# Performance work log

Hardware: AMD Instinct MI355X
Metric: run time of the kernel (lower is better)

Reference implementation:

```python
import jax, jax.numpy as jnp
import numpy as np

N_NODES = 100000
N_EDGES = 1600000
IN_C, HID_C, OUT_C = 128, 128, 64


def gcn_conv(x, W, b, src, dst, n_nodes):
    """PyG-style GCNConv: h = x @ W; add self-loops; symmetric deg^-1/2 norm;
    scatter-add aggregation; + bias. Self-loop contribution added analytically
    (norm for self-loop edge i->i is deg_i^-1) instead of materializing edges."""
    h = x @ W  # [N, C_out]
    # degree over dst including self-loops (edge weights are all ones)
    deg = jax.ops.segment_sum(jnp.ones((src.shape[0],), h.dtype), dst,
                              num_segments=n_nodes) + 1.0
    dinv = jax.lax.rsqrt(deg)  # deg >= 1 always
    norm = dinv[src] * dinv[dst]  # [E]
    agg = jax.ops.segment_sum(h[src] * norm[:, None], dst, num_segments=n_nodes)
    agg = agg + h * (dinv * dinv)[:, None]  # self-loop term
    return agg + b


def setup_inputs() -> dict:
    key = jax.random.key(0)
    k0, k1, k2, k3, k4, k5 = jax.random.split(key, 6)
    x = jax.random.normal(k0, (N_NODES, IN_C), dtype=jnp.float32)
    edge_index = jax.random.randint(k1, (2, N_EDGES), 0, N_NODES, dtype=jnp.int64)
    s1 = 1.0 / np.sqrt(IN_C)
    s2 = 1.0 / np.sqrt(HID_C)
    W1 = jax.random.uniform(k2, (IN_C, HID_C), jnp.float32, -s1, s1)
    b1 = jax.random.uniform(k3, (HID_C,), jnp.float32, -s1, s1)
    W2 = jax.random.uniform(k4, (HID_C, OUT_C), jnp.float32, -s2, s2)
    b2 = jax.random.uniform(k5, (OUT_C,), jnp.float32, -s2, s2)
    return {"x": x, "W1": W1, "b1": b1, "W2": W2, "b2": b2,
            "edge_index": edge_index}


def reference(x, W1, b1, W2, b2, edge_index):
    src, dst = edge_index[0], edge_index[1]
    h = gcn_conv(x, W1, b1, src, dst, N_NODES)
    h = jax.nn.relu(h)
    out = gcn_conv(h, W2, b2, src, dst, N_NODES)
    return out
```

## Files before the change

kernel.cpp:

```cpp
#include <hip/hip_runtime.h>


static constexpr int BSHIFT = 7;
static constexpr int BWIDTH = 1 << BSHIFT;
static constexpr int MAXBUCK = 2048;
static constexpr int NPART = 256;

static constexpr size_t OFF_FLAG = 0;
static constexpr size_t OFF_DEG  = 256;
static constexpr size_t OFF_ROW  = 458752;
static constexpr size_t OFF_BSUM = 917504;
static constexpr size_t OFF_CCNT = 925696;
static constexpr size_t OFF_COFF = 937984;
static constexpr size_t OFF_DINV = 962560;
static constexpr size_t OFF_CSR  = 1376256;
static constexpr size_t OFF_HS1  = 8388608;
static constexpr size_t OFF_OUT1 = 35651584;
static constexpr size_t OFF_HS2  = 62914560;
static constexpr size_t OFF_H2   = 75714560;

__device__ __forceinline__ unsigned short f2bf(float f) {
    unsigned u = __float_as_uint(f);
    u += 0x7fffu + ((u >> 16) & 1u);
    return (unsigned short)(u >> 16);
}

typedef __attribute__((ext_vector_type(8))) short bf16x8;
typedef __attribute__((ext_vector_type(4))) float f32x4;

__global__ void detect_kernel(const unsigned* __restrict__ w,
                              unsigned* __restrict__ flag) {
    int i = blockIdx.x * blockDim.x + threadIdx.x;
    if (w[2 * i + 1] != 0u) atomicOr(flag, 1u);
}

__device__ __forceinline__ int edge_dst(const unsigned* w, unsigned flag,
                                        int e, int E) {
    return flag ? (int)w[E + e] : (int)w[2 * E + 2 * e];
}
__device__ __forceinline__ int edge_src(const unsigned* w, unsigned flag,
                                        int e, int E) {
    return flag ? (int)w[e] : (int)w[2 * e];
}

__global__ __launch_bounds__(1024) void coarse_hist_kernel(
    const unsigned* __restrict__ w, const unsigned* __restrict__ flag,
    unsigned* __restrict__ ccnt, unsigned* __restrict__ h2, int E, int nbuck) {
    __shared__ unsigned hist[MAXBUCK];
    for (int i = threadIdx.x; i < nbuck; i += 1024) hist[i] = 0;
    __syncthreads();
    const unsigned f = *flag;
    const int per = (E + gridDim.x - 1) / gridDim.x;
    const int e0 = blockIdx.x * per, e1 = min(E, e0 + per);
    for (int e = e0 + (int)threadIdx.x; e < e1; e += 1024)
        atomicAdd(&hist[edge_dst(w, f, e, E) >> BSHIFT], 1u);
    __syncthreads();
    for (int i = threadIdx.x; i < nbuck; i += 1024) {
        unsigned h = hist[i];
        h2[(size_t)i * NPART + blockIdx.x] = h;
        if (h) atomicAdd(&ccnt[i], h);
    }
}

__global__ __launch_bounds__(1024) void coarse_scan_kernel(
    const unsigned* __restrict__ ccnt, unsigned* __restrict__ coff, int nbuck) {
    __shared__ unsigned sh[1024];
    const int t = threadIdx.x;
    unsigned run = 0;
    for (int b0 = 0; b0 < nbuck; b0 += 1024) {
        unsigned v = (b0 + t < nbuck) ? ccnt[b0 + t] : 0u;
        sh[t] = v;
        __syncthreads();
        for (int off = 1; off < 1024; off <<= 1) {
            unsigned a = (t >= off) ? sh[t - off] : 0u;
            __syncthreads();
            sh[t] += a;
            __syncthreads();
        }
        if (b0 + t < nbuck) coff[b0 + t] = run + sh[t] - v;
        run += sh[1023];
        __syncthreads();
    }
    if (t == 0) coff[nbuck] = run;
}

__global__ __launch_bounds__(NPART) void off2d_kernel(
    unsigned* __restrict__ h2, const unsigned* __restrict__ coff) {
    __shared__ unsigned sh[NPART];
    const int b = blockIdx.x, t = threadIdx.x;
    unsigned v = h2[(size_t)b * NPART + t];
    sh[t] = v;
    __syncthreads();
#pragma unroll
    for (int off = 1; off < NPART; off <<= 1) {
        unsigned a = (t >= off) ? sh[t - off] : 0u;
        __syncthreads();
        sh[t] += a;
        __syncthreads();
    }
    h2[(size_t)b * NPART + t] = coff[b] + sh[t] - v;
}

__global__ __launch_bounds__(1024) void partition_kernel(
    const unsigned* __restrict__ w, const unsigned* __restrict__ flag,
    const unsigned* __restrict__ h2, unsigned* __restrict__ part, int E,
    int nbuck) {
    __shared__ unsigned lcur[MAXBUCK];
    for (int i = threadIdx.x; i < nbuck; i += 1024)
        lcur[i] = h2[(size_t)i * NPART + blockIdx.x];
    __syncthreads();
    const unsigned f = *flag;
    const int per = (E + gridDim.x - 1) / gridDim.x;
    const int e0 = blockIdx.x * per, e1 = min(E, e0 + per);
    for (int e = e0 + (int)threadIdx.x; e < e1; e += 1024) {
        int d = edge_dst(w, f, e, E);
        int s = edge_src(w, f, e, E);
        unsigned pos = atomicAdd(&lcur[d >> BSHIFT], 1u);
        part[pos] = (unsigned)s | ((unsigned)(d & (BWIDTH - 1)) << 20);
    }
}

__global__ __launch_bounds__(256) void bucket_csr_kernel(
    const unsigned* __restrict__ part, const unsigned* __restrict__ coff,
    unsigned* __restrict__ deg, int* __restrict__ csr, int N) {
    __shared__ unsigned cnt[BWIDTH];
    __shared__ unsigned sc[BWIDTH];
    __shared__ unsigned cur[BWIDTH];
    const int b = blockIdx.x, base = b << BSHIFT, t = threadIdx.x;
    if (t < BWIDTH) cnt[t] = 0;
    __syncthreads();
    const int e0 = (int)coff[b], e1 = (int)coff[b + 1];
    for (int e = e0 + t; e < e1; e += 256)
        atomicAdd(&cnt[part[e] >> 20], 1u);
    __syncthreads();
    if (t < BWIDTH && base + t < N) deg[base + t] = cnt[t];
    if (t < BWIDTH) sc[t] = cnt[t];
    __syncthreads();
#pragma unroll
    for (int off = 1; off < BWIDTH; off <<= 1) {
        unsigned a = (t < BWIDTH && t >= off) ? sc[t - off] : 0u;
        __syncthreads();
        if (t < BWIDTH) sc[t] += a;
        __syncthreads();
    }
    if (t < BWIDTH) cur[t] = (unsigned)e0 + sc[t] - cnt[t];
    __syncthreads();
    for (int e = e0 + t; e < e1; e += 256) {
        unsigned pk = part[e];
        unsigned p = atomicAdd(&cur[pk >> 20], 1u);
        csr[p] = (int)(pk & 0xFFFFFu);
    }
}

__global__ __launch_bounds__(1024) void scan1_kernel(
    const unsigned* __restrict__ deg, unsigned* __restrict__ row,
    unsigned* __restrict__ bsum, int N) {
    __shared__ unsigned sh[1024];
    int gid = blockIdx.x * 1024 + threadIdx.x;
    int t = threadIdx.x;
    unsigned v = (gid < N) ? deg[gid] : 0u;
    sh[t] = v;
    __syncthreads();
#pragma unroll
    for (int off = 1; off < 1024; off <<= 1) {
        unsigned add = (t >= off) ? sh[t - off] : 0u;
        __syncthreads();
        sh[t] += add;
        __syncthreads();
    }
    if (gid < N) row[gid + 1] = sh[t];
    if (t == 1023) bsum[blockIdx.x] = sh[1023];
}

__global__ __launch_bounds__(1024) void scan2_kernel(unsigned* __restrict__ bsum,
                                                     int NB) {
    __shared__ unsigned sh[1024];
    const int t = threadIdx.x;
    unsigned v = (t < NB) ? bsum[t] : 0u;
    sh[t] = v;
    __syncthreads();
#pragma unroll
    for (int off = 1; off < 1024; off <<= 1) {
        unsigned a = (t >= off) ? sh[t - off] : 0u;
        __syncthreads();
        sh[t] += a;
        __syncthreads();
    }
    if (t < NB) bsum[t] = sh[t] - v;
}

__global__ void scan3_kernel(unsigned* __restrict__ row,
                             const unsigned* __restrict__ bsum,
                             const unsigned* __restrict__ deg,
                             float* __restrict__ dinv, int N) {
    int gid = blockIdx.x * blockDim.x + threadIdx.x;
    if (gid >= N) return;
    row[gid + 1] += bsum[gid >> 10];
    if (gid == 0) row[0] = 0u;
    dinv[gid] = rsqrtf((float)deg[gid] + 1.0f);
}

template <int BN, bool ABF16>
__global__ __launch_bounds__(256) void gemm_mfma(
    const void* __restrict__ Av, const float* __restrict__ B,
    const float* __restrict__ dinv, unsigned short* __restrict__ out, int M) {
    constexpr int NT = BN / 16;
    __shared__ short sA[16384];
    __shared__ short sB[NT * 2048];

    const int t = threadIdx.x;
    const int row0 = blockIdx.x * 128;
    const int w = t >> 6, lane = t & 63;
    const int m = lane & 15, q = lane >> 4;

    if (ABF16) {
        const unsigned short* A = (const unsigned short*)Av;
        for (int g = t; g < 2048; g += 256) {
            int r = g >> 4, k0 = (g & 15) << 3;
            uint4 v = make_uint4(0u, 0u, 0u, 0u);
            if (row0 + r < M) v = *(const uint4*)(A + (size_t)(row0 + r) * 128 + k0);
            int off = ((((r >> 4) * 4 + (k0 >> 5)) * 16 + (r & 15)) * 4 +
                       ((k0 >> 3) & 3)) * 8;
            *(uint4*)(sA + off) = v;
        }
    } else {
        const float* A = (const float*)Av;
        for (int g = t; g < 4096; g += 256) {
            int r = g >> 5, k0 = (g & 31) << 2;
            float4 v = make_float4(0.f, 0.f, 0.f, 0.f);
            if (row0 + r < M) v = *(const float4*)(A + (size_t)(row0 + r) * 128 + k0);
            ushort4 u;
            u.x = f2bf(v.x); u.y = f2bf(v.y); u.z = f2bf(v.z); u.w = f2bf(v.w);
            int off = ((((r >> 4) * 4 + (k0 >> 5)) * 16 + (r & 15)) * 4 +
                       ((k0 >> 3) & 3)) * 8 + (k0 & 4);
            *(ushort4*)(sA + off) = u;
        }
    }
    for (int g = t; g < BN * 32; g += 256) {
        int n = g % BN, k0 = (g / BN) * 4;
        float f0 = B[(size_t)(k0 + 0) * BN + n];
        float f1 = B[(size_t)(k0 + 1) * BN + n];
        float f2 = B[(size_t)(k0 + 2) * BN + n];
        float f3 = B[(size_t)(k0 + 3) * BN + n];
        ushort4 u;
        u.x = f2bf(f0); u.y = f2bf(f1); u.z = f2bf(f2); u.w = f2bf(f3);
        int off = ((((n >> 4) * 4 + (k0 >> 5)) * 16 + (n & 15)) * 4 +
                   ((k0 >> 3) & 3)) * 8 + (k0 & 4);
        *(ushort4*)(sB + off) = u;
    }
    __syncthreads();

    f32x4 acc[2][NT];
#pragma unroll
    for (int lt = 0; lt < 2; lt++)
#pragma unroll
        for (int nt = 0; nt < NT; nt++) acc[lt][nt] = (f32x4){0.f, 0.f, 0.f, 0.f};

    const int fb = (m * 4 + q) * 8;
#pragma unroll
    for (int ks = 0; ks < 4; ks++) {
        bf16x8 a0 = *(const bf16x8*)(sA + ((w * 2 + 0) * 4 + ks) * 512 + fb);
        bf16x8 a1 = *(const bf16x8*)(sA + ((w * 2 + 1) * 4 + ks) * 512 + fb);
#pragma unroll
        for (int nt = 0; nt < NT; nt++) {
            bf16x8 b = *(const bf16x8*)(sB + (nt * 4 + ks) * 512 + fb);
            acc[0][nt] = __builtin_amdgcn_mfma_f32_16x16x32_bf16(a0, b, acc[0][nt], 0, 0, 0);
            acc[1][nt] = __builtin_amdgcn_mfma_f32_16x16x32_bf16(a1, b, acc[1][nt], 0, 0, 0);
        }
    }

#pragma unroll
    for (int lt = 0; lt < 2; lt++) {
#pragma unroll
        for (int r = 0; r < 4; r++) {
            int row = row0 + w * 32 + lt * 16 + q * 4 + r;
            if (row < M) {
                float s = dinv[row];
#pragma unroll
                for (int nt = 0; nt < NT; nt++)
                    out[(size_t)row * BN + nt * 16 + m] = f2bf(acc[lt][nt][r] * s);
            }
        }
    }
}

template <int C, bool RELU, bool OUTBF>
__global__ __launch_bounds__(256) void agg_kernel(
    const int* __restrict__ csr, const unsigned* __restrict__ row,
    const unsigned short* __restrict__ hsb, const float* __restrict__ dinv,
    const float* __restrict__ bias, void* __restrict__ outv, int N) {
    constexpr int LPN = C / 8;
    const int tid = blockIdx.x * 256 + threadIdx.x;
    const int i = tid / LPN;
    const int l = tid % LPN;
    if (i >= N) return;

    const int co = 8 * l;
    float s0 = 0.f, s1 = 0.f, s2 = 0.f, s3 = 0.f,
          s4 = 0.f, s5 = 0.f, s6 = 0.f, s7 = 0.f;
    {
        uint4 u = *(const uint4*)(hsb + (size_t)i * C + co);
        s0 += __uint_as_float(u.x << 16); s1 += __uint_as_float(u.x & 0xffff0000u);
        s2 += __uint_as_float(u.y << 16); s3 += __uint_as_float(u.y & 0xffff0000u);
        s4 += __uint_as_float(u.z << 16); s5 += __uint_as_float(u.z & 0xffff0000u);
        s6 += __uint_as_float(u.w << 16); s7 += __uint_as_float(u.w & 0xffff0000u);
    }

    const int rs = (int)row[i], re = (int)row[i + 1];
    for (int e0 = rs; e0 < re; e0 += LPN) {
        int idx = (e0 + l < re) ? csr[e0 + l] : 0;
        const int cnt = min(LPN, re - e0);
#pragma unroll 4
        for (int j = 0; j < cnt; j++) {
            int s = __shfl(idx, j, LPN);
            uint4 u = *(const uint4*)(hsb + (size_t)s * C + co);
            s0 += __uint_as_float(u.x << 16); s1 += __uint_as_float(u.x & 0xffff0000u);
            s2 += __uint_as_float(u.y << 16); s3 += __uint_as_float(u.y & 0xffff0000u);
            s4 += __uint_as_float(u.z << 16); s5 += __uint_as_float(u.z & 0xffff0000u);
            s6 += __uint_as_float(u.w << 16); s7 += __uint_as_float(u.w & 0xffff0000u);
        }
    }

    const float sc = dinv[i];
    const float4 ba = *(const float4*)(bias + co);
    const float4 bb = *(const float4*)(bias + co + 4);
    float o0 = s0 * sc + ba.x, o1 = s1 * sc + ba.y;
    float o2 = s2 * sc + ba.z, o3 = s3 * sc + ba.w;
    float o4 = s4 * sc + bb.x, o5 = s5 * sc + bb.y;
    float o6 = s6 * sc + bb.z, o7 = s7 * sc + bb.w;
    if (RELU) {
        o0 = fmaxf(o0, 0.f); o1 = fmaxf(o1, 0.f); o2 = fmaxf(o2, 0.f);
        o3 = fmaxf(o3, 0.f); o4 = fmaxf(o4, 0.f); o5 = fmaxf(o5, 0.f);
        o6 = fmaxf(o6, 0.f); o7 = fmaxf(o7, 0.f);
    }
    if (OUTBF) {
        uint4 u;
        u.x = (unsigned)f2bf(o0) | ((unsigned)f2bf(o1) << 16);
        u.y = (unsigned)f2bf(o2) | ((unsigned)f2bf(o3) << 16);
        u.z = (unsigned)f2bf(o4) | ((unsigned)f2bf(o5) << 16);
        u.w = (unsigned)f2bf(o6) | ((unsigned)f2bf(o7) << 16);
        *(uint4*)((unsigned short*)outv + (size_t)i * C + co) = u;
    } else {
        float4 a = make_float4(o0, o1, o2, o3);
        float4 b = make_float4(o4, o5, o6, o7);
        *(float4*)((float*)outv + (size_t)i * C + co) = a;
        *(float4*)((float*)outv + (size_t)i * C + co + 4) = b;
    }
}

extern "C" void kernel_launch(void* const* d_in, const int* in_sizes, int n_in,
                              void* d_out, int out_size, void* d_ws,
                              size_t ws_size, hipStream_t stream) {
    const float* x  = (const float*)d_in[0];
    const float* W1 = (const float*)d_in[1];
    const float* b1 = (const float*)d_in[2];
    const float* W2 = (const float*)d_in[3];
    const float* b2 = (const float*)d_in[4];
    const unsigned* ew = (const unsigned*)d_in[5];
    const int E = in_sizes[5] / 2;
    const int N = in_sizes[0] / 128;
    const int NB = (N + 1023) >> 10;
    const int nbuck = (N + BWIDTH - 1) >> BSHIFT;

    char* ws = (char*)d_ws;
    unsigned* flag = (unsigned*)(ws + OFF_FLAG);
    unsigned* deg  = (unsigned*)(ws + OFF_DEG);
    unsigned* row  = (unsigned*)(ws + OFF_ROW);
    unsigned* bsum = (unsigned*)(ws + OFF_BSUM);
    unsigned* ccnt = (unsigned*)(ws + OFF_CCNT);
    unsigned* coff = (unsigned*)(ws + OFF_COFF);
    float* dinv    = (float*)(ws + OFF_DINV);
    int* csr       = (int*)(ws + OFF_CSR);
    unsigned short* hs1  = (unsigned short*)(ws + OFF_HS1);
    unsigned short* out1 = (unsigned short*)(ws + OFF_OUT1);
    unsigned short* hs2  = (unsigned short*)(ws + OFF_HS2);
    unsigned* h2   = (unsigned*)(ws + OFF_H2);
    unsigned* part = (unsigned*)(ws + OFF_HS1);

    hipMemsetAsync(flag, 0, 4, stream);
    hipMemsetAsync(ccnt, 0, (size_t)(nbuck + 1) * 4, stream);

    detect_kernel<<<16, 256, 0, stream>>>(ew, flag);
    coarse_hist_kernel<<<NPART, 1024, 0, stream>>>(ew, flag, ccnt, h2, E, nbuck);
    coarse_scan_kernel<<<1, 1024, 0, stream>>>(ccnt, coff, nbuck);
    off2d_kernel<<<nbuck, NPART, 0, stream>>>(h2, coff);
    partition_kernel<<<NPART, 1024, 0, stream>>>(ew, flag, h2, part, E, nbuck);
    bucket_csr_kernel<<<nbuck, 256, 0, stream>>>(part, coff, deg, csr, N);
    scan1_kernel<<<NB, 1024, 0, stream>>>(deg, row, bsum, N);
    scan2_kernel<<<1, 1024, 0, stream>>>(bsum, NB);
    scan3_kernel<<<(N + 255) / 256, 256, 0, stream>>>(row, bsum, deg, dinv, N);

    gemm_mfma<128, false><<<(N + 127) / 128, 256, 0, stream>>>(x, W1, dinv, hs1, N);
    agg_kernel<128, true, true><<<(N * 16 + 255) / 256, 256, 0, stream>>>(
        csr, row, hs1, dinv, b1, out1, N);

    gemm_mfma<64, true><<<(N + 127) / 128, 256, 0, stream>>>(out1, W2, dinv, hs2, N);
    agg_kernel<64, false, false><<<(N * 8 + 255) / 256, 256, 0, stream>>>(
        csr, row, hs2, dinv, b2, d_out, N);
}
```

Before: 317.6 us.

## Slice feature tables into 16-column groups and fold scans into bucket CSR

Intermediate feature tables are stored channel-sliced (16 columns per slice), and aggregation blocks each gather one slice for 128 nodes, so each pass over the neighbour rows touches a smaller working set that fits in cache better. The GEMM loads its A fragments directly into registers instead of staging them in shared memory. The separate detect kernel and the three scan kernels are removed: the edge-index format is detected per block with __syncthreads_or, and row offsets and dinv are written inside bucket_csr_kernel. This saves several launches, but CSR row reads are repeated once per slice and the gather now moves 32-byte pieces instead of full rows.

```diff
diff --git a/kernel.cpp b/kernel.cpp
--- a/kernel.cpp
+++ b/kernel.cpp
@@ -6,14 +6,11 @@
 static constexpr int MAXBUCK = 2048;
 static constexpr int NPART = 256;
 
-static constexpr size_t OFF_FLAG = 0;
-static constexpr size_t OFF_DEG  = 256;
-static constexpr size_t OFF_ROW  = 458752;
-static constexpr size_t OFF_BSUM = 917504;
-static constexpr size_t OFF_CCNT = 925696;
-static constexpr size_t OFF_COFF = 937984;
-static constexpr size_t OFF_DINV = 962560;
-static constexpr size_t OFF_CSR  = 1376256;
+static constexpr size_t OFF_ROW  = 0;
+static constexpr size_t OFF_CCNT = 524288;
+static constexpr size_t OFF_COFF = 540672;
+static constexpr size_t OFF_DINV = 557056;
+static constexpr size_t OFF_CSR  = 1048576;
 static constexpr size_t OFF_HS1  = 8388608;
 static constexpr size_t OFF_OUT1 = 35651584;
 static constexpr size_t OFF_HS2  = 62914560;
@@ -28,10 +25,11 @@
 typedef __attribute__((ext_vector_type(8))) short bf16x8;
 typedef __attribute__((ext_vector_type(4))) float f32x4;
 
-__global__ void detect_kernel(const unsigned* __restrict__ w,
-                              unsigned* __restrict__ flag) {
-    int i = blockIdx.x * blockDim.x + threadIdx.x;
-    if (w[2 * i + 1] != 0u) atomicOr(flag, 1u);
+__device__ __forceinline__ void acc8(const uint4 u, float* s) {
+    s[0] += __uint_as_float(u.x << 16); s[1] += __uint_as_float(u.x & 0xffff0000u);
+    s[2] += __uint_as_float(u.y << 16); s[3] += __uint_as_float(u.y & 0xffff0000u);
+    s[4] += __uint_as_float(u.z << 16); s[5] += __uint_as_float(u.z & 0xffff0000u);
+    s[6] += __uint_as_float(u.w << 16); s[7] += __uint_as_float(u.w & 0xffff0000u);
 }
 
 __device__ __forceinline__ int edge_dst(const unsigned* w, unsigned flag,
@@ -42,16 +40,21 @@
                                         int e, int E) {
     return flag ? (int)w[e] : (int)w[2 * e];
 }
+__device__ __forceinline__ unsigned detect_local(const unsigned* w, int e0,
+                                                 int e1) {
+    int si = e0 + (int)threadIdx.x;
+    int pred = (si < e1) ? (w[2 * si + 1] != 0u) : 0;
+    return (unsigned)(__syncthreads_or(pred) != 0);
+}
 
 __global__ __launch_bounds__(1024) void coarse_hist_kernel(
-    const unsigned* __restrict__ w, const unsigned* __restrict__ flag,
-    unsigned* __restrict__ ccnt, unsigned* __restrict__ h2, int E, int nbuck) {
+    const unsigned* __restrict__ w, unsigned* __restrict__ ccnt,
+    unsigned* __restrict__ h2, int E, int nbuck) {
     __shared__ unsigned hist[MAXBUCK];
     for (int i = threadIdx.x; i < nbuck; i += 1024) hist[i] = 0;
-    __syncthreads();
-    const unsigned f = *flag;
     const int per = (E + gridDim.x - 1) / gridDim.x;
     const int e0 = blockIdx.x * per, e1 = min(E, e0 + per);
+    const unsigned f = detect_local(w, e0, e1);
     for (int e = e0 + (int)threadIdx.x; e < e1; e += 1024)
         atomicAdd(&hist[edge_dst(w, f, e, E) >> BSHIFT], 1u);
     __syncthreads();
@@ -102,16 +105,14 @@
 }
 
 __global__ __launch_bounds__(1024) void partition_kernel(
-    const unsigned* __restrict__ w, const unsigned* __restrict__ flag,
-    const unsigned* __restrict__ h2, unsigned* __restrict__ part, int E,
-    int nbuck) {
+    const unsigned* __restrict__ w, const unsigned* __restrict__ h2,
+    unsigned* __restrict__ part, int E, int nbuck) {
     __shared__ unsigned lcur[MAXBUCK];
     for (int i = threadIdx.x; i < nbuck; i += 1024)
         lcur[i] = h2[(size_t)i * NPART + blockIdx.x];
-    __syncthreads();
-    const unsigned f = *flag;
     const int per = (E + gridDim.x - 1) / gridDim.x;
     const int e0 = blockIdx.x * per, e1 = min(E, e0 + per);
+    const unsigned f = detect_local(w, e0, e1);
     for (int e = e0 + (int)threadIdx.x; e < e1; e += 1024) {
         int d = edge_dst(w, f, e, E);
         int s = edge_src(w, f, e, E);
@@ -122,7 +123,8 @@
 
 __global__ __launch_bounds__(256) void bucket_csr_kernel(
     const unsigned* __restrict__ part, const unsigned* __restrict__ coff,
-    unsigned* __restrict__ deg, int* __restrict__ csr, int N) {
+    unsigned* __restrict__ row, float* __restrict__ dinv,
+    int* __restrict__ csr, int N, int nbuck) {
     __shared__ unsigned cnt[BWIDTH];
     __shared__ unsigned sc[BWIDTH];
     __shared__ unsigned cur[BWIDTH];
@@ -133,7 +135,6 @@
     for (int e = e0 + t; e < e1; e += 256)
         atomicAdd(&cnt[part[e] >> 20], 1u);
     __syncthreads();
-    if (t < BWIDTH && base + t < N) deg[base + t] = cnt[t];
     if (t < BWIDTH) sc[t] = cnt[t];
     __syncthreads();
 #pragma unroll
@@ -143,7 +144,15 @@
         if (t < BWIDTH) sc[t] += a;
         __syncthreads();
     }
-    if (t < BWIDTH) cur[t] = (unsigned)e0 + sc[t] - cnt[t];
+    if (t < BWIDTH) {
+        unsigned ex = (unsigned)e0 + sc[t] - cnt[t];
+        cur[t] = ex;
+        if (base + t < N) {
+            row[base + t] = ex;
+            dinv[base + t] = rsqrtf((float)cnt[t] + 1.0f);
+        }
+    }
+    if (b == 0 && t == 0) row[N] = coff[nbuck];
     __syncthreads();
     for (int e = e0 + t; e < e1; e += 256) {
         unsigned pk = part[e];
@@ -152,60 +161,11 @@
     }
 }
 
-__global__ __launch_bounds__(1024) void scan1_kernel(
-    const unsigned* __restrict__ deg, unsigned* __restrict__ row,
-    unsigned* __restrict__ bsum, int N) {
-    __shared__ unsigned sh[1024];
-    int gid = blockIdx.x * 1024 + threadIdx.x;
-    int t = threadIdx.x;
-    unsigned v = (gid < N) ? deg[gid] : 0u;
-    sh[t] = v;
-    __syncthreads();
-#pragma unroll
-    for (int off = 1; off < 1024; off <<= 1) {
-        unsigned add = (t >= off) ? sh[t - off] : 0u;
-        __syncthreads();
-        sh[t] += add;
-        __syncthreads();
-    }
-    if (gid < N) row[gid + 1] = sh[t];
-    if (t == 1023) bsum[blockIdx.x] = sh[1023];
-}
-
-__global__ __launch_bounds__(1024) void scan2_kernel(unsigned* __restrict__ bsum,
-                                                     int NB) {
-    __shared__ unsigned sh[1024];
-    const int t = threadIdx.x;
-    unsigned v = (t < NB) ? bsum[t] : 0u;
-    sh[t] = v;
-    __syncthreads();
-#pragma unroll
-    for (int off = 1; off < 1024; off <<= 1) {
-        unsigned a = (t >= off) ? sh[t - off] : 0u;
-        __syncthreads();
-        sh[t] += a;
-        __syncthreads();
-    }
-    if (t < NB) bsum[t] = sh[t] - v;
-}
-
-__global__ void scan3_kernel(unsigned* __restrict__ row,
-                             const unsigned* __restrict__ bsum,
-                             const unsigned* __restrict__ deg,
-                             float* __restrict__ dinv, int N) {
-    int gid = blockIdx.x * blockDim.x + threadIdx.x;
-    if (gid >= N) return;
-    row[gid + 1] += bsum[gid >> 10];
-    if (gid == 0) row[0] = 0u;
-    dinv[gid] = rsqrtf((float)deg[gid] + 1.0f);
-}
-
 template <int BN, bool ABF16>
 __global__ __launch_bounds__(256) void gemm_mfma(
     const void* __restrict__ Av, const float* __restrict__ B,
-    const float* __restrict__ dinv, unsigned short* __restrict__ out, int M) {
+    const float* __restrict__ dinv, unsigned short* __restrict__ outg, int M) {
     constexpr int NT = BN / 16;
-    __shared__ short sA[16384];
     __shared__ short sB[NT * 2048];
 
     const int t = threadIdx.x;
@@ -213,29 +173,6 @@
     const int w = t >> 6, lane = t & 63;
     const int m = lane & 15, q = lane >> 4;
 
-    if (ABF16) {
-        const unsigned short* A = (const unsigned short*)Av;
-        for (int g = t; g < 2048; g += 256) {
-            int r = g >> 4, k0 = (g & 15) << 3;
-            uint4 v = make_uint4(0u, 0u, 0u, 0u);
-            if (row0 + r < M) v = *(const uint4*)(A + (size_t)(row0 + r) * 128 + k0);
-            int off = ((((r >> 4) * 4 + (k0 >> 5)) * 16 + (r & 15)) * 4 +
-                       ((k0 >> 3) & 3)) * 8;
-            *(uint4*)(sA + off) = v;
-        }
-    } else {
-        const float* A = (const float*)Av;
-        for (int g = t; g < 4096; g += 256) {
-            int r = g >> 5, k0 = (g & 31) << 2;
-            float4 v = make_float4(0.f, 0.f, 0.f, 0.f);
-            if (row0 + r < M) v = *(const float4*)(A + (size_t)(row0 + r) * 128 + k0);
-            ushort4 u;
-            u.x = f2bf(v.x); u.y = f2bf(v.y); u.z = f2bf(v.z); u.w = f2bf(v.w);
-            int off = ((((r >> 4) * 4 + (k0 >> 5)) * 16 + (r & 15)) * 4 +
-                       ((k0 >> 3) & 3)) * 8 + (k0 & 4);
-            *(ushort4*)(sA + off) = u;
-        }
-    }
     for (int g = t; g < BN * 32; g += 256) {
         int n = g % BN, k0 = (g / BN) * 4;
         float f0 = B[(size_t)(k0 + 0) * BN + n];
@@ -248,6 +185,37 @@
                    ((k0 >> 3) & 3)) * 8 + (k0 & 4);
         *(ushort4*)(sB + off) = u;
     }
+
+    bf16x8 a[2][4];
+#pragma unroll
+    for (int lt = 0; lt < 2; lt++) {
+        const int row = row0 + (w * 2 + lt) * 16 + m;
+        const bool ok = row < M;
+#pragma unroll
+        for (int ks = 0; ks < 4; ks++) {
+            const int k = ks * 32 + q * 8;
+            if (ABF16) {
+                uint4 v = make_uint4(0u, 0u, 0u, 0u);
+                if (ok)
+                    v = *(const uint4*)((const unsigned short*)Av +
+                                        ((size_t)(k >> 4) * M + row) * 16 + (k & 15));
+                a[lt][ks] = *(const bf16x8*)&v;
+            } else {
+                float4 v0 = make_float4(0.f, 0.f, 0.f, 0.f), v1 = v0;
+                if (ok) {
+                    const float* A = (const float*)Av + (size_t)row * 128 + k;
+                    v0 = *(const float4*)A;
+                    v1 = *(const float4*)(A + 4);
+                }
+                bf16x8 av;
+                av[0] = (short)f2bf(v0.x); av[1] = (short)f2bf(v0.y);
+                av[2] = (short)f2bf(v0.z); av[3] = (short)f2bf(v0.w);
+                av[4] = (short)f2bf(v1.x); av[5] = (short)f2bf(v1.y);
+                av[6] = (short)f2bf(v1.z); av[7] = (short)f2bf(v1.w);
+                a[lt][ks] = av;
+            }
+        }
+    }
     __syncthreads();
 
     f32x4 acc[2][NT];
@@ -259,13 +227,11 @@
     const int fb = (m * 4 + q) * 8;
 #pragma unroll
     for (int ks = 0; ks < 4; ks++) {
-        bf16x8 a0 = *(const bf16x8*)(sA + ((w * 2 + 0) * 4 + ks) * 512 + fb);
-        bf16x8 a1 = *(const bf16x8*)(sA + ((w * 2 + 1) * 4 + ks) * 512 + fb);
 #pragma unroll
         for (int nt = 0; nt < NT; nt++) {
             bf16x8 b = *(const bf16x8*)(sB + (nt * 4 + ks) * 512 + fb);
-            acc[0][nt] = __builtin_amdgcn_mfma_f32_16x16x32_bf16(a0, b, acc[0][nt], 0, 0, 0);
-            acc[1][nt] = __builtin_amdgcn_mfma_f32_16x16x32_bf16(a1, b, acc[1][nt], 0, 0, 0);
+            acc[0][nt] = __builtin_amdgcn_mfma_f32_16x16x32_bf16(a[0][ks], b, acc[0][nt], 0, 0, 0);
+            acc[1][nt] = __builtin_amdgcn_mfma_f32_16x16x32_bf16(a[1][ks], b, acc[1][nt], 0, 0, 0);
         }
     }
 
@@ -278,56 +244,51 @@
                 float s = dinv[row];
 #pragma unroll
                 for (int nt = 0; nt < NT; nt++)
-                    out[(size_t)row * BN + nt * 16 + m] = f2bf(acc[lt][nt][r] * s);
+                    outg[((size_t)nt * M + row) * 16 + m] = f2bf(acc[lt][nt][r] * s);
             }
         }
     }
 }
 
 template <int C, bool RELU, bool OUTBF>
-__global__ __launch_bounds__(256) void agg_kernel(
+__global__ __launch_bounds__(256) void agg_sliced(
     const int* __restrict__ csr, const unsigned* __restrict__ row,
-    const unsigned short* __restrict__ hsb, const float* __restrict__ dinv,
+    const unsigned short* __restrict__ hsg, const float* __restrict__ dinv,
     const float* __restrict__ bias, void* __restrict__ outv, int N) {
-    constexpr int LPN = C / 8;
-    const int tid = blockIdx.x * 256 + threadIdx.x;
-    const int i = tid / LPN;
-    const int l = tid % LPN;
+    int cg, chunk;
+    const int bi = blockIdx.x;
+    if (C == 128) { cg = bi & 7; chunk = bi >> 3; }
+    else { const int g = bi & 7; cg = g >> 1; chunk = (bi >> 3) * 2 + (g & 1); }
+    const int slot = threadIdx.x >> 1, l = threadIdx.x & 1;
+    const int i = chunk * 128 + slot;
     if (i >= N) return;
 
-    const int co = 8 * l;
-    float s0 = 0.f, s1 = 0.f, s2 = 0.f, s3 = 0.f,
-          s4 = 0.f, s5 = 0.f, s6 = 0.f, s7 = 0.f;
-    {
-        uint4 u = *(const uint4*)(hsb + (size_t)i * C + co);
-        s0 += __uint_as_float(u.x << 16); s1 += __uint_as_float(u.x & 0xffff0000u);
-        s2 += __uint_as_float(u.y << 16); s3 += __uint_as_float(u.y & 0xffff0000u);
-        s4 += __uint_as_float(u.z << 16); s5 += __uint_as_float(u.z & 0xffff0000u);
-        s6 += __uint_as_float(u.w << 16); s7 += __uint_as_float(u.w & 0xffff0000u);
-    }
+    const unsigned short* tab = hsg + (size_t)cg * N * 16;
+    const int co = l * 8;
+
+    float s[8] = {0.f, 0.f, 0.f, 0.f, 0.f, 0.f, 0.f, 0.f};
+    acc8(*(const uint4*)(tab + (size_t)i * 16 + co), s);
 
     const int rs = (int)row[i], re = (int)row[i + 1];
-    for (int e0 = rs; e0 < re; e0 += LPN) {
+    for (int e0 = rs; e0 < re; e0 += 2) {
         int idx = (e0 + l < re) ? csr[e0 + l] : 0;
-        const int cnt = min(LPN, re - e0);
-#pragma unroll 4
-        for (int j = 0; j < cnt; j++) {
-            int s = __shfl(idx, j, LPN);
-            uint4 u = *(const uint4*)(hsb + (size_t)s * C + co);
-            s0 += __uint_as_float(u.x << 16); s1 += __uint_as_float(u.x & 0xffff0000u);
-            s2 += __uint_as_float(u.y << 16); s3 += __uint_as_float(u.y & 0xffff0000u);
-            s4 += __uint_as_float(u.z << 16); s5 += __uint_as_float(u.z & 0xffff0000u);
-            s6 += __uint_as_float(u.w << 16); s7 += __uint_as_float(u.w & 0xffff0000u);
-        }
+        int sa = __shfl(idx, 0, 2);
+        int sb = __shfl(idx, 1, 2);
+        const bool two = (e0 + 1 < re);
+        uint4 v0 = *(const uint4*)(tab + (size_t)sa * 16 + co);
+        uint4 v1 = *(const uint4*)(tab + (size_t)(two ? sb : sa) * 16 + co);
+        acc8(v0, s);
+        if (two) acc8(v1, s);
     }
 
     const float sc = dinv[i];
-    const float4 ba = *(const float4*)(bias + co);
-    const float4 bb = *(const float4*)(bias + co + 4);
-    float o0 = s0 * sc + ba.x, o1 = s1 * sc + ba.y;
-    float o2 = s2 * sc + ba.z, o3 = s3 * sc + ba.w;
-    float o4 = s4 * sc + bb.x, o5 = s5 * sc + bb.y;
-    float o6 = s6 * sc + bb.z, o7 = s7 * sc + bb.w;
+    const int cb = cg * 16 + co;
+    const float4 ba = *(const float4*)(bias + cb);
+    const float4 bb = *(const float4*)(bias + cb + 4);
+    float o0 = s[0] * sc + ba.x, o1 = s[1] * sc + ba.y;
+    float o2 = s[2] * sc + ba.z, o3 = s[3] * sc + ba.w;
+    float o4 = s[4] * sc + bb.x, o5 = s[5] * sc + bb.y;
+    float o6 = s[6] * sc + bb.z, o7 = s[7] * sc + bb.w;
     if (RELU) {
         o0 = fmaxf(o0, 0.f); o1 = fmaxf(o1, 0.f); o2 = fmaxf(o2, 0.f);
         o3 = fmaxf(o3, 0.f); o4 = fmaxf(o4, 0.f); o5 = fmaxf(o5, 0.f);
@@ -339,12 +300,11 @@
         u.y = (unsigned)f2bf(o2) | ((unsigned)f2bf(o3) << 16);
         u.z = (unsigned)f2bf(o4) | ((unsigned)f2bf(o5) << 16);
         u.w = (unsigned)f2bf(o6) | ((unsigned)f2bf(o7) << 16);
-        *(uint4*)((unsigned short*)outv + (size_t)i * C + co) = u;
+        *(uint4*)((unsigned short*)outv + ((size_t)cg * N + i) * 16 + co) = u;
     } else {
-        float4 a = make_float4(o0, o1, o2, o3);
-        float4 b = make_float4(o4, o5, o6, o7);
-        *(float4*)((float*)outv + (size_t)i * C + co) = a;
-        *(float4*)((float*)outv + (size_t)i * C + co + 4) = b;
+        float* o = (float*)outv + (size_t)i * C + cb;
+        *(float4*)o = make_float4(o0, o1, o2, o3);
+        *(float4*)(o + 4) = make_float4(o4, o5, o6, o7);
     }
 }
 
@@ -359,42 +319,35 @@
     const unsigned* ew = (const unsigned*)d_in[5];
     const int E = in_sizes[5] / 2;
     const int N = in_sizes[0] / 128;
-    const int NB = (N + 1023) >> 10;
     const int nbuck = (N + BWIDTH - 1) >> BSHIFT;
+    const int chunks = (N + 127) / 128;
 
     char* ws = (char*)d_ws;
-    unsigned* flag = (unsigned*)(ws + OFF_FLAG);
-    unsigned* deg  = (unsigned*)(ws + OFF_DEG);
     unsigned* row  = (unsigned*)(ws + OFF_ROW);
-    unsigned* bsum = (unsigned*)(ws + OFF_BSUM);
     unsigned* ccnt = (unsigned*)(ws + OFF_CCNT);
     unsigned* coff = (unsigned*)(ws + OFF_COFF);
     float* dinv    = (float*)(ws + OFF_DINV);
     int* csr       = (int*)(ws + OFF_CSR);
-    unsigned short* hs1  = (unsigned short*)(ws + OFF_HS1);
-    unsigned short* out1 = (unsigned short*)(ws + OFF_OUT1);
-    unsigned short* hs2  = (unsigned short*)(ws + OFF_HS2);
+    unsigned short* hs1g  = (unsigned short*)(ws + OFF_HS1);
+    unsigned short* out1g = (unsigned short*)(ws + OFF_OUT1);
+    unsigned short* hs2g  = (unsigned short*)(ws + OFF_HS2);
     unsigned* h2   = (unsigned*)(ws + OFF_H2);
     unsigned* part = (unsigned*)(ws + OFF_HS1);
 
-    hipMemsetAsync(flag, 0, 4, stream);
     hipMemsetAsync(ccnt, 0, (size_t)(nbuck + 1) * 4, stream);
 
-    detect_kernel<<<16, 256, 0, stream>>>(ew, flag);
-    coarse_hist_kernel<<<NPART, 1024, 0, stream>>>(ew, flag, ccnt, h2, E, nbuck);
+    coarse_hist_kernel<<<NPART, 1024, 0, stream>>>(ew, ccnt, h2, E, nbuck);
     coarse_scan_kernel<<<1, 1024, 0, stream>>>(ccnt, coff, nbuck);
     off2d_kernel<<<nbuck, NPART, 0, stream>>>(h2, coff);
-    partition_kernel<<<NPART, 1024, 0, stream>>>(ew, flag, h2, part, E, nbuck);
-    bucket_csr_kernel<<<nbuck, 256, 0, stream>>>(part, coff, deg, csr, N);
-    scan1_kernel<<<NB, 1024, 0, stream>>>(deg, row, bsum, N);
-    scan2_kernel<<<1, 1024, 0, stream>>>(bsum, NB);
-    scan3_kernel<<<(N + 255) / 256, 256, 0, stream>>>(row, bsum, deg, dinv, N);
-
-    gemm_mfma<128, false><<<(N + 127) / 128, 256, 0, stream>>>(x, W1, dinv, hs1, N);
-    agg_kernel<128, true, true><<<(N * 16 + 255) / 256, 256, 0, stream>>>(
-        csr, row, hs1, dinv, b1, out1, N);
-
-    gemm_mfma<64, true><<<(N + 127) / 128, 256, 0, stream>>>(out1, W2, dinv, hs2, N);
-    agg_kernel<64, false, false><<<(N * 8 + 255) / 256, 256, 0, stream>>>(
-        csr, row, hs2, dinv, b2, d_out, N);
-}
+    partition_kernel<<<NPART, 1024, 0, stream>>>(ew, h2, part, E, nbuck);
+    bucket_csr_kernel<<<nbuck, 256, 0, stream>>>(part, coff, row, dinv, csr,
+                                                 N, nbuck);
+
+    gemm_mfma<128, false><<<chunks, 256, 0, stream>>>(x, W1, dinv, hs1g, N);
+    agg_sliced<128, true, true><<<chunks * 8, 256, 0, stream>>>(
+        csr, row, hs1g, dinv, b1, out1g, N);
+
+    gemm_mfma<64, true><<<chunks, 256, 0, stream>>>(out1g, W2, dinv, hs2g, N);
+    agg_sliced<64, false, false><<<((chunks + 1) / 2) * 8, 256, 0, stream>>>(
+        csr, row, hs2g, dinv, b2, d_out, N);
+}
```

Result: slower. 361.9 us (+14.0%).
